# Optimization experiments

Measured on AMD Instinct MI355X. Metric: run time of the kernel, lower is better.

## Reference

```python
import jax, jax.numpy as jnp
import numpy as np


def squash(s):
    # v = (|s|^2 / (1 + |s|^2)) * s / |s|, norm over last axis
    sn = jnp.sum(s * s, axis=-1, keepdims=True)
    return sn / (1.0 + sn) * s / jnp.sqrt(sn)


def setup_inputs() -> dict:
    key = jax.random.key(0)
    k1, k2, k3 = jax.random.split(key, 3)
    N, C, D, W, H = 32, 32, 16, 16, 16
    K, P = 10, 4
    l = jax.random.normal(k1, (N, C, D, W, H), dtype=jnp.float32)
    g = jax.random.normal(k2, (N, K, D), dtype=jnp.float32)
    weight = jax.random.normal(k3, (1, C, 1, K, P, P), dtype=jnp.float32)
    return {"l": l, "g": g, "weight": weight, "n_rout": 3}


def reference(l, g, weight, n_rout):
    N, C, D, W, H = l.shape
    K = weight.shape[3]
    P = weight.shape[-1]  # D == P*P
    # (N,C,D,W,H) -> (N,C,W*H,P,P)
    lr = jnp.transpose(l, (0, 1, 3, 4, 2)).reshape(N, C, W * H, P, P)
    # per-capsule 4x4 vote matmul against per-(channel,class) weight
    wt = weight[0, :, 0]  # (C,K,P,P)
    V = jnp.einsum('ncsij,ckjd->ncskid', lr, wt)  # (N,C,S,K,P,P)
    B = C * W * H
    V = V.reshape(N, B, K, P * P)  # (N,B,K,D) votes
    # initial logits from global capsule g: b = <g, V> over D
    b = jnp.sum(g[:, None, :, :] * V, axis=-1, keepdims=True)  # (N,B,K,1)
    gc = None
    for _ in range(n_rout):
        c = jax.nn.softmax(b, axis=2)                 # softmax over classes K
        s = jnp.sum(V * c, axis=1, keepdims=True)     # (N,1,K,D)
        gc = squash(s)                                # (N,1,K,D)
        b = jnp.sum(gc * V, axis=-1, keepdims=True)   # (N,B,K,1)
    a = jax.nn.sigmoid(jnp.sqrt(jnp.sum(gc * gc, axis=-1)))  # (N,1,K)
    return a.reshape(N, K), gc.reshape(N, K, P * P)
```

## Files before the change

kernel.cpp:

```cpp
#include <hip/hip_runtime.h>


#define KK 10
#define PP 16
#define CC 32
#define SS 256
#define NN 32
#define RR 3
#define GR 4
#define BPN 8

__global__ __launch_bounds__(1024, 4) void fused_kernel(
    const float* __restrict__ l,
    const float* __restrict__ w,
    const float* __restrict__ g,
    float* __restrict__ s_buf,
    int*   __restrict__ ctr,
    float* __restrict__ out_a,
    float* __restrict__ out_gc)
{
  const int bid = blockIdx.x;
  const int n   = bid >> 3;
  const int cg  = bid & 7;
  const int t   = threadIdx.x;
  const int grp = t >> 8;
  const int tt  = t & 255;
  const int c   = cg * GR + grp;

  __shared__ float lr_lds[GR][PP][SS + 4];
  __shared__ float ct_lds[GR][KK][SS + 4];
  __shared__ float w_lds[GR][KK * PP];
  __shared__ float U_lds[GR][KK * PP];
  __shared__ float pmerge[GR][4][KK * PP];
  __shared__ float sred[GR][KK * PP];
  __shared__ float gc_lds[KK * PP];
  __shared__ float f_lds[KK];

  if (tt < KK * PP) w_lds[grp][tt] = w[c * KK * PP + tt];
  float lr[PP];
  const float* lb = l + (size_t)(n * CC + c) * (PP * SS) + tt;
  #pragma unroll
  for (int d = 0; d < PP; ++d) {
    lr[d] = lb[d * SS];
    lr_lds[grp][d][tt] = lr[d];
  }
  if (t < KK * PP) gc_lds[t] = g[n * KK * PP + t];
  __syncthreads();

  #pragma unroll 1
  for (int r = 0; r < RR; ++r) {
    if (r > 0) {
      if (t < KK) {
        float sn = 0.f;
        #pragma unroll
        for (int m = 0; m < PP; ++m) { const float v = gc_lds[t * PP + m]; sn += v * v; }
        f_lds[t] = sn / (1.f + sn) * rsqrtf(sn);
      }
      __syncthreads();
      if (t < KK * PP) gc_lds[t] *= f_lds[t >> 4];
      __syncthreads();
    }

    if (tt < KK * PP) {
      const int k = tt >> 4, ij = tt & 15, i = ij >> 2, j = ij & 3;
      const float4 wv = *(const float4*)&w_lds[grp][k * PP + j * 4];
      const float4 gv = *(const float4*)&gc_lds[k * PP + i * 4];
      U_lds[grp][tt] = wv.x * gv.x + wv.y * gv.y + wv.z * gv.z + wv.w * gv.w;
    }
    __syncthreads();

    {
      float b[KK];
      float bmax = -1e30f;
      #pragma unroll
      for (int k = 0; k < KK; ++k) {
        float acc = 0.f;
        #pragma unroll
        for (int d4 = 0; d4 < 4; ++d4) {
          const float4 uv = *(const float4*)&U_lds[grp][k * PP + d4 * 4];
          acc += lr[d4*4+0]*uv.x + lr[d4*4+1]*uv.y + lr[d4*4+2]*uv.z + lr[d4*4+3]*uv.w;
        }
        b[k] = acc;
        bmax = fmaxf(bmax, acc);
      }
      float ssum = 0.f;
      #pragma unroll
      for (int k = 0; k < KK; ++k) { b[k] = __expf(b[k] - bmax); ssum += b[k]; }
      const float inv = 1.f / ssum;
      #pragma unroll
      for (int k = 0; k < KK; ++k) ct_lds[grp][k][tt] = b[k] * inv;
    }
    __syncthreads();

    {
      const int ch = tt >> 4, ij = tt & 15, sbase = ch * 16;
      float acc[KK];
      #pragma unroll
      for (int k = 0; k < KK; ++k) acc[k] = 0.f;
      #pragma unroll
      for (int s4 = 0; s4 < 4; ++s4) {
        const float4 lv = *(const float4*)&lr_lds[grp][ij][sbase + s4 * 4];
        #pragma unroll
        for (int k = 0; k < KK; ++k) {
          const float4 cv = *(const float4*)&ct_lds[grp][k][sbase + s4 * 4];
          acc[k] += cv.x*lv.x + cv.y*lv.y + cv.z*lv.z + cv.w*lv.w;
        }
      }
      #pragma unroll
      for (int k = 0; k < KK; ++k) {
        acc[k] += __shfl_xor(acc[k], 16);
        acc[k] += __shfl_xor(acc[k], 32);
      }
      const int wv = tt >> 6;
      if ((tt & 63) < 16) {
        #pragma unroll
        for (int k = 0; k < KK; ++k) pmerge[grp][wv][k * PP + ij] = acc[k];
      }
    }
    __syncthreads();

    if (tt < KK * PP) {
      U_lds[grp][tt] = pmerge[grp][0][tt] + pmerge[grp][1][tt]
                     + pmerge[grp][2][tt] + pmerge[grp][3][tt];
    }
    __syncthreads();

    if (tt < KK * PP) {
      const int k = tt >> 4, i = (tt >> 2) & 3, d = tt & 3;
      const float* Mp  = &U_lds[grp][k * PP + i * 4];
      const float* wpt = &w_lds[grp][k * PP + d];
      sred[grp][tt] = Mp[0]*wpt[0] + Mp[1]*wpt[4] + Mp[2]*wpt[8] + Mp[3]*wpt[12];
    }
    __syncthreads();

    float* s_r = s_buf + (size_t)r * NN * KK * PP;
    if (t < KK * PP) {
      atomicAdd(&s_r[n * KK * PP + t],
                sred[0][t] + sred[1][t] + sred[2][t] + sred[3][t]);
    }
    __syncthreads();

    if (t == 0)
      __hip_atomic_fetch_add(&ctr[r * NN + n], 1,
                             __ATOMIC_RELEASE, __HIP_MEMORY_SCOPE_AGENT);

    if (r < RR - 1) {
      if (t == 0) {
        int guard = 0;
        while (__hip_atomic_load(&ctr[r * NN + n],
                                 __ATOMIC_RELAXED, __HIP_MEMORY_SCOPE_AGENT) < BPN
               && ++guard < (1 << 24))
          __builtin_amdgcn_s_sleep(2);
      }
      __syncthreads();
      if (t < KK * PP)
        gc_lds[t] = __hip_atomic_load(&s_r[n * KK * PP + t],
                                      __ATOMIC_RELAXED, __HIP_MEMORY_SCOPE_AGENT);
      __syncthreads();
    }
  }

  if (cg == 0) {
    float* s2 = s_buf + (size_t)2 * NN * KK * PP;
    if (t == 0) {
      int guard = 0;
      while (__hip_atomic_load(&ctr[2 * NN + n],
                               __ATOMIC_RELAXED, __HIP_MEMORY_SCOPE_AGENT) < BPN
             && ++guard < (1 << 24))
        __builtin_amdgcn_s_sleep(2);
    }
    __syncthreads();
    if (t < KK * PP)
      gc_lds[t] = __hip_atomic_load(&s2[n * KK * PP + t],
                                    __ATOMIC_RELAXED, __HIP_MEMORY_SCOPE_AGENT);
    __syncthreads();
    if (t < KK) {
      float sn = 0.f;
      #pragma unroll
      for (int m = 0; m < PP; ++m) { const float v = gc_lds[t * PP + m]; sn += v * v; }
      f_lds[t] = sn / (1.f + sn) * rsqrtf(sn);
      const float gn = sn / (1.f + sn);
      out_a[n * KK + t] = 1.f / (1.f + __expf(-gn));
    }
    __syncthreads();
    if (t < KK * PP) out_gc[n * KK * PP + t] = gc_lds[t] * f_lds[t >> 4];
  }
}

extern "C" void kernel_launch(void* const* d_in, const int* in_sizes, int n_in,
                              void* d_out, int out_size, void* d_ws, size_t ws_size,
                              hipStream_t stream) {
  const float* l = (const float*)d_in[0];
  const float* g = (const float*)d_in[1];
  const float* w = (const float*)d_in[2];

  float* out    = (float*)d_out;
  float* out_a  = out;
  float* out_gc = out + NN * KK;

  float* s_buf = (float*)d_ws;
  int*   ctr   = (int*)((char*)d_ws +
                        (size_t)3 * NN * KK * PP * sizeof(float));
  const size_t zero_bytes =
      (size_t)3 * NN * KK * PP * sizeof(float) + (size_t)3 * NN * sizeof(int);
  hipMemsetAsync(d_ws, 0, zero_bytes, stream);

  fused_kernel<<<NN * BPN, 1024, 0, stream>>>(l, w, g, s_buf, ctr,
                                              out_a, out_gc);
}
```

Baseline: 101.0 us.

## Split work to one block per channel with fixed-point 64-bit atomic reduction

Each block now handles one (batch, channel) pair with 256 threads instead of four channels per 1024-thread block. This gives 1024 blocks and removes the in-block cross-group reduction. The cross-block sum over channels now uses 64-bit integer atomics on fixed-point values, which makes the result deterministic, in place of float atomicAdd. The costs are 4x more global atomics per batch, and each per-batch spin barrier now waits on 32 blocks instead of 8. That raises contention and the risk of deadlock if not all blocks are co-resident.

```diff
diff --git a/kernel.cpp b/kernel.cpp
--- a/kernel.cpp
+++ b/kernel.cpp
@@ -7,44 +7,43 @@
 #define SS 256
 #define NN 32
 #define RR 3
-#define GR 4
-#define BPN 8
-
-__global__ __launch_bounds__(1024, 4) void fused_kernel(
+#define SE (KK * PP)
+
+typedef unsigned long long u64;
+#define SCALE_F  4294967296.0f
+#define INV_SCALE (1.0 / 4294967296.0)
+
+__global__ __launch_bounds__(256, 4) void fused_kernel(
     const float* __restrict__ l,
     const float* __restrict__ w,
     const float* __restrict__ g,
-    float* __restrict__ s_buf,
+    u64*   __restrict__ s_buf,
     int*   __restrict__ ctr,
     float* __restrict__ out_a,
     float* __restrict__ out_gc)
 {
   const int bid = blockIdx.x;
-  const int n   = bid >> 3;
-  const int cg  = bid & 7;
-  const int t   = threadIdx.x;
-  const int grp = t >> 8;
-  const int tt  = t & 255;
-  const int c   = cg * GR + grp;
-
-  __shared__ float lr_lds[GR][PP][SS + 4];
-  __shared__ float ct_lds[GR][KK][SS + 4];
-  __shared__ float w_lds[GR][KK * PP];
-  __shared__ float U_lds[GR][KK * PP];
-  __shared__ float pmerge[GR][4][KK * PP];
-  __shared__ float sred[GR][KK * PP];
-  __shared__ float gc_lds[KK * PP];
+  const int n = bid >> 5;
+  const int c = bid & 31;
+  const int t = threadIdx.x;
+
+  __shared__ float lr_lds[PP][SS + 4];
+  __shared__ float ct_lds[KK][SS + 4];
+  __shared__ float U_lds[SE];
+  __shared__ float w_lds[SE];
+  __shared__ float gc_lds[SE];
   __shared__ float f_lds[KK];
-
-  if (tt < KK * PP) w_lds[grp][tt] = w[c * KK * PP + tt];
+  __shared__ float pmerge[4][SE];
+
+  if (t < SE) w_lds[t] = w[c * SE + t];
   float lr[PP];
-  const float* lb = l + (size_t)(n * CC + c) * (PP * SS) + tt;
+  const float* lb = l + (size_t)(n * CC + c) * (PP * SS) + t;
   #pragma unroll
   for (int d = 0; d < PP; ++d) {
     lr[d] = lb[d * SS];
-    lr_lds[grp][d][tt] = lr[d];
+    lr_lds[d][t] = lr[d];
   }
-  if (t < KK * PP) gc_lds[t] = g[n * KK * PP + t];
+  if (t < SE) gc_lds[t] = g[n * SE + t];
   __syncthreads();
 
   #pragma unroll 1
@@ -57,15 +56,15 @@
         f_lds[t] = sn / (1.f + sn) * rsqrtf(sn);
       }
       __syncthreads();
-      if (t < KK * PP) gc_lds[t] *= f_lds[t >> 4];
-      __syncthreads();
-    }
-
-    if (tt < KK * PP) {
-      const int k = tt >> 4, ij = tt & 15, i = ij >> 2, j = ij & 3;
-      const float4 wv = *(const float4*)&w_lds[grp][k * PP + j * 4];
+      if (t < SE) gc_lds[t] *= f_lds[t >> 4];
+      __syncthreads();
+    }
+
+    if (t < SE) {
+      const int k = t >> 4, ij = t & 15, i = ij >> 2, j = ij & 3;
+      const float4 wv = *(const float4*)&w_lds[k * PP + j * 4];
       const float4 gv = *(const float4*)&gc_lds[k * PP + i * 4];
-      U_lds[grp][tt] = wv.x * gv.x + wv.y * gv.y + wv.z * gv.z + wv.w * gv.w;
+      U_lds[t] = wv.x * gv.x + wv.y * gv.y + wv.z * gv.z + wv.w * gv.w;
     }
     __syncthreads();
 
@@ -77,7 +76,7 @@
         float acc = 0.f;
         #pragma unroll
         for (int d4 = 0; d4 < 4; ++d4) {
-          const float4 uv = *(const float4*)&U_lds[grp][k * PP + d4 * 4];
+          const float4 uv = *(const float4*)&U_lds[k * PP + d4 * 4];
           acc += lr[d4*4+0]*uv.x + lr[d4*4+1]*uv.y + lr[d4*4+2]*uv.z + lr[d4*4+3]*uv.w;
         }
         b[k] = acc;
@@ -88,21 +87,21 @@
       for (int k = 0; k < KK; ++k) { b[k] = __expf(b[k] - bmax); ssum += b[k]; }
       const float inv = 1.f / ssum;
       #pragma unroll
-      for (int k = 0; k < KK; ++k) ct_lds[grp][k][tt] = b[k] * inv;
+      for (int k = 0; k < KK; ++k) ct_lds[k][t] = b[k] * inv;
     }
     __syncthreads();
 
     {
-      const int ch = tt >> 4, ij = tt & 15, sbase = ch * 16;
+      const int ch = t >> 4, ij = t & 15, sbase = ch * 16;
       float acc[KK];
       #pragma unroll
       for (int k = 0; k < KK; ++k) acc[k] = 0.f;
       #pragma unroll
       for (int s4 = 0; s4 < 4; ++s4) {
-        const float4 lv = *(const float4*)&lr_lds[grp][ij][sbase + s4 * 4];
+        const float4 lv = *(const float4*)&lr_lds[ij][sbase + s4 * 4];
         #pragma unroll
         for (int k = 0; k < KK; ++k) {
-          const float4 cv = *(const float4*)&ct_lds[grp][k][sbase + s4 * 4];
+          const float4 cv = *(const float4*)&ct_lds[k][sbase + s4 * 4];
           acc[k] += cv.x*lv.x + cv.y*lv.y + cv.z*lv.z + cv.w*lv.w;
         }
       }
@@ -111,32 +110,27 @@
         acc[k] += __shfl_xor(acc[k], 16);
         acc[k] += __shfl_xor(acc[k], 32);
       }
-      const int wv = tt >> 6;
-      if ((tt & 63) < 16) {
-        #pragma unroll
-        for (int k = 0; k < KK; ++k) pmerge[grp][wv][k * PP + ij] = acc[k];
-      }
-    }
-    __syncthreads();
-
-    if (tt < KK * PP) {
-      U_lds[grp][tt] = pmerge[grp][0][tt] + pmerge[grp][1][tt]
-                     + pmerge[grp][2][tt] + pmerge[grp][3][tt];
-    }
-    __syncthreads();
-
-    if (tt < KK * PP) {
-      const int k = tt >> 4, i = (tt >> 2) & 3, d = tt & 3;
-      const float* Mp  = &U_lds[grp][k * PP + i * 4];
-      const float* wpt = &w_lds[grp][k * PP + d];
-      sred[grp][tt] = Mp[0]*wpt[0] + Mp[1]*wpt[4] + Mp[2]*wpt[8] + Mp[3]*wpt[12];
-    }
-    __syncthreads();
-
-    float* s_r = s_buf + (size_t)r * NN * KK * PP;
-    if (t < KK * PP) {
-      atomicAdd(&s_r[n * KK * PP + t],
-                sred[0][t] + sred[1][t] + sred[2][t] + sred[3][t]);
+      const int wv = t >> 6;
+      if ((t & 63) < 16) {
+        #pragma unroll
+        for (int k = 0; k < KK; ++k) pmerge[wv][k * PP + ij] = acc[k];
+      }
+    }
+    __syncthreads();
+
+    if (t < SE) {
+      U_lds[t] = pmerge[0][t] + pmerge[1][t] + pmerge[2][t] + pmerge[3][t];
+    }
+    __syncthreads();
+
+    u64* s_r = s_buf + (size_t)r * NN * SE;
+    if (t < SE) {
+      const int k = t >> 4, i = (t >> 2) & 3, d = t & 3;
+      const float* Mp  = U_lds + k * PP + i * 4;
+      const float* wpt = w_lds + k * PP + d;
+      const float sv = Mp[0]*wpt[0] + Mp[1]*wpt[4] + Mp[2]*wpt[8] + Mp[3]*wpt[12];
+      const long long q = llrintf(sv * SCALE_F);
+      atomicAdd(&s_r[n * SE + t], (u64)q);
     }
     __syncthreads();
 
@@ -148,31 +142,35 @@
       if (t == 0) {
         int guard = 0;
         while (__hip_atomic_load(&ctr[r * NN + n],
-                                 __ATOMIC_RELAXED, __HIP_MEMORY_SCOPE_AGENT) < BPN
+                                 __ATOMIC_RELAXED, __HIP_MEMORY_SCOPE_AGENT) < CC
                && ++guard < (1 << 24))
           __builtin_amdgcn_s_sleep(2);
       }
       __syncthreads();
-      if (t < KK * PP)
-        gc_lds[t] = __hip_atomic_load(&s_r[n * KK * PP + t],
-                                      __ATOMIC_RELAXED, __HIP_MEMORY_SCOPE_AGENT);
+      if (t < SE) {
+        const u64 v = __hip_atomic_load(&s_r[n * SE + t],
+                                        __ATOMIC_RELAXED, __HIP_MEMORY_SCOPE_AGENT);
+        gc_lds[t] = (float)((double)(long long)v * INV_SCALE);
+      }
       __syncthreads();
     }
   }
 
-  if (cg == 0) {
-    float* s2 = s_buf + (size_t)2 * NN * KK * PP;
+  if (c == 0) {
+    u64* s2 = s_buf + (size_t)2 * NN * SE;
     if (t == 0) {
       int guard = 0;
       while (__hip_atomic_load(&ctr[2 * NN + n],
-                               __ATOMIC_RELAXED, __HIP_MEMORY_SCOPE_AGENT) < BPN
+                               __ATOMIC_RELAXED, __HIP_MEMORY_SCOPE_AGENT) < CC
              && ++guard < (1 << 24))
         __builtin_amdgcn_s_sleep(2);
     }
     __syncthreads();
-    if (t < KK * PP)
-      gc_lds[t] = __hip_atomic_load(&s2[n * KK * PP + t],
-                                    __ATOMIC_RELAXED, __HIP_MEMORY_SCOPE_AGENT);
+    if (t < SE) {
+      const u64 v = __hip_atomic_load(&s2[n * SE + t],
+                                      __ATOMIC_RELAXED, __HIP_MEMORY_SCOPE_AGENT);
+      gc_lds[t] = (float)((double)(long long)v * INV_SCALE);
+    }
     __syncthreads();
     if (t < KK) {
       float sn = 0.f;
@@ -183,7 +181,7 @@
       out_a[n * KK + t] = 1.f / (1.f + __expf(-gn));
     }
     __syncthreads();
-    if (t < KK * PP) out_gc[n * KK * PP + t] = gc_lds[t] * f_lds[t >> 4];
+    if (t < SE) out_gc[n * SE + t] = gc_lds[t] * f_lds[t >> 4];
   }
 }
 
@@ -198,13 +196,11 @@
   float* out_a  = out;
   float* out_gc = out + NN * KK;
 
-  float* s_buf = (float*)d_ws;
-  int*   ctr   = (int*)((char*)d_ws +
-                        (size_t)3 * NN * KK * PP * sizeof(float));
-  const size_t zero_bytes =
-      (size_t)3 * NN * KK * PP * sizeof(float) + (size_t)3 * NN * sizeof(int);
-  hipMemsetAsync(d_ws, 0, zero_bytes, stream);
-
-  fused_kernel<<<NN * BPN, 1024, 0, stream>>>(l, w, g, s_buf, ctr,
-                                              out_a, out_gc);
+  u64* s_buf = (u64*)d_ws;
+  const size_t s_bytes = (size_t)RR * NN * SE * sizeof(u64);
+  int* ctr   = (int*)((char*)d_ws + s_bytes);
+  hipMemsetAsync(d_ws, 0, s_bytes + (size_t)RR * NN * sizeof(int), stream);
+
+  fused_kernel<<<NN * CC, 256, 0, stream>>>(l, w, g, s_buf, ctr,
+                                            out_a, out_gc);
 }
```

Result: slower. 211.2 us (+109.1%).
